# Kernel optimization log

Hardware: AMD Instinct MI355X
Metric: run time of the kernel (lower is better)

The kernel has to match this reference:

```python
import jax, jax.numpy as jnp
import numpy as np

BN_EPS = 1e-5

def conv1x1(x, w, b):
    # x: [B, Cin, L], w: [Cout, Cin], b: [Cout] -> [B, Cout, L]
    return jnp.einsum('bcl,oc->bol', x, w) + b[None, :, None]

def maxpool2(x):
    # x: [B, C, L] -> [B, C, L//2], kernel=stride=2
    B, C, L = x.shape
    return x.reshape(B, C, L // 2, 2).max(axis=-1)

def setup_inputs() -> dict:
    key = jax.random.key(0)
    ks = jax.random.split(key, 12)
    B, C, L = 8, 512, 4096
    Ci = C // 2
    s_in = 1.0 / np.sqrt(C)
    s_mid = 1.0 / np.sqrt(Ci)
    return {
        'x':       jax.random.normal(ks[0], (B, C, L), jnp.float32),
        'theta_w': jax.random.uniform(ks[1], (Ci, C), jnp.float32, -s_in, s_in),
        'theta_b': jax.random.uniform(ks[2], (Ci,), jnp.float32, -s_in, s_in),
        'phi_w':   jax.random.uniform(ks[3], (Ci, C), jnp.float32, -s_in, s_in),
        'phi_b':   jax.random.uniform(ks[4], (Ci,), jnp.float32, -s_in, s_in),
        'g_w':     jax.random.uniform(ks[5], (Ci, C), jnp.float32, -s_in, s_in),
        'g_b':     jax.random.uniform(ks[6], (Ci,), jnp.float32, -s_in, s_in),
        'wz_w':    jax.random.uniform(ks[7], (C, Ci), jnp.float32, -s_mid, s_mid),
        'wz_b':    jax.random.uniform(ks[8], (C,), jnp.float32, -s_mid, s_mid),
        'bn_gamma': jax.random.normal(ks[9], (C,), jnp.float32),
        'bn_beta':  jax.random.normal(ks[10], (C,), jnp.float32),
    }

def reference(x, theta_w, theta_b, phi_w, phi_b, g_w, g_b, wz_w, wz_b, bn_gamma, bn_beta):
    B, C, L = x.shape
    Ci = C // 2
    # projections
    theta = conv1x1(x, theta_w, theta_b)                 # [B, Ci, L]
    phi   = maxpool2(conv1x1(x, phi_w, phi_b))           # [B, Ci, L/2]
    g     = maxpool2(conv1x1(x, g_w, g_b))               # [B, Ci, L/2]
    # non-local attention (unscaled)
    f = jnp.einsum('bcq,bck->bqk', theta, phi)           # [B, L, L/2]
    f = jax.nn.softmax(f, axis=-1)
    y = jnp.einsum('bqk,bck->bcq', f, g)                 # [B, Ci, L]
    # wz: conv1x1 + BatchNorm1d (training mode: batch stats, biased var)
    z = conv1x1(y, wz_w, wz_b)                           # [B, C, L]
    mean = z.mean(axis=(0, 2))
    var = ((z - mean[None, :, None]) ** 2).mean(axis=(0, 2))
    z_hat = (z - mean[None, :, None]) * jax.lax.rsqrt(var + BN_EPS)[None, :, None]
    wz = z_hat * bn_gamma[None, :, None] + bn_beta[None, :, None]
    return wz + x
```

## Files before the change

kernel.cpp:

```cpp
#include <hip/hip_runtime.h>

#define BATCH 8
#define CIN   512
#define LEN   4096
#define CI    256
#define KLEN  2048

typedef _Float16 half_t;
typedef _Float16 half2_t __attribute__((ext_vector_type(2)));
typedef _Float16 half4_t __attribute__((ext_vector_type(4)));
typedef _Float16 half8_t __attribute__((ext_vector_type(8)));
typedef float    floatx4 __attribute__((ext_vector_type(4)));

__device__ __forceinline__ void async16(void* lds_dst, const void* g_src) {
    __builtin_amdgcn_global_load_lds(
        (const __attribute__((address_space(1))) unsigned int*)g_src,
        (__attribute__((address_space(3))) unsigned int*)lds_dst,
        16, 0, 0);
}

__global__ __launch_bounds__(256) void xpose_kernel(
    const float* __restrict__ x, half_t* __restrict__ xhT)
{
    __shared__ half_t tile[64][72];
    const int b = blockIdx.z, c0 = blockIdx.y * 64, l0 = blockIdx.x * 64;
    const int t = threadIdx.x;
    #pragma unroll
    for (int i = 0; i < 4; i++) {
        int fid = t + 256 * i;
        int c = fid >> 4, lb = (fid & 15) << 2;
        float4 v = *(const float4*)(x + ((size_t)b * CIN + c0 + c) * LEN + l0 + lb);
        tile[lb + 0][c] = (half_t)v.x;
        tile[lb + 1][c] = (half_t)v.y;
        tile[lb + 2][c] = (half_t)v.z;
        tile[lb + 3][c] = (half_t)v.w;
    }
    __syncthreads();
    #pragma unroll
    for (int i = 0; i < 2; i++) {
        int fid = t + 256 * i;
        int l = fid >> 3, cb = (fid & 7) << 3;
        half8_t v = *(const half8_t*)&tile[l][cb];
        *(half8_t*)(xhT + ((size_t)b * LEN + l0 + l) * CIN + c0 + cb) = v;
    }
}

__global__ __launch_bounds__(256) void wconv_kernel(
    const float* __restrict__ tw, const float* __restrict__ pw,
    const float* __restrict__ gw, const float* __restrict__ wzw,
    half_t* __restrict__ Wh, half_t* __restrict__ wzh)
{
    size_t base = ((size_t)blockIdx.x * 256 + threadIdx.x) * 8;
    const float* src;
    half_t* dst;
    if (base < 768 * 512) {
        size_t o = base >> 9, c = base & 511;
        src = (o < 256 ? tw + o * 512
                       : (o < 512 ? pw + (o - 256) * 512 : gw + (o - 512) * 512)) + c;
        dst = Wh + base;
    } else {
        size_t off = base - 768 * 512;
        src = wzw + off;
        dst = wzh + off;
    }
    float4 a = *(const float4*)src, b2 = *(const float4*)(src + 4);
    half8_t h = { (half_t)a.x, (half_t)a.y, (half_t)a.z, (half_t)a.w,
                  (half_t)b2.x, (half_t)b2.y, (half_t)b2.z, (half_t)b2.w };
    *(half8_t*)dst = h;
}

__global__ __launch_bounds__(256, 2) void projmm_kernel(
    const half_t* __restrict__ xhT, const half_t* __restrict__ Wh,
    const float* __restrict__ tb, const float* __restrict__ pb,
    const float* __restrict__ gb,
    half_t* __restrict__ thetaT, half_t* __restrict__ phiT,
    half_t* __restrict__ gH)
{
    __shared__ half_t wsm[128 * 32];
    __shared__ half_t xsm[128 * 32];

    const int b  = blockIdx.z;
    const int o0 = blockIdx.y * 128;
    const int l0 = blockIdx.x * 128;
    const int t  = threadIdx.x;
    const int lane = t & 63, w = t >> 6;
    const int ln = lane & 15, quad = lane >> 4;
    const int wm = w >> 1, wn = w & 1;

    floatx4 acc[4][4];
    #pragma unroll
    for (int mi = 0; mi < 4; mi++)
        #pragma unroll
        for (int nj = 0; nj < 4; nj++) acc[mi][nj] = (floatx4)(0.0f);

    const half_t* Wb = Wh + (size_t)o0 * 512;
    const half_t* xb = xhT + ((size_t)b * LEN + l0) * CIN;

    for (int k0 = 0; k0 < 512; k0 += 32) {
        __syncthreads();
        #pragma unroll
        for (int it = 0; it < 2; it++) {
            int off = t * 16 + it * 4096;
            int row = off >> 6, c8 = (off >> 4) & 3;
            async16(&wsm[off >> 1], Wb + (size_t)row * 512 + k0 + c8 * 8);
            async16(&xsm[off >> 1], xb + (size_t)row * CIN + k0 + c8 * 8);
        }
        __syncthreads();
        half8_t af[4], bf[4];
        #pragma unroll
        for (int mi = 0; mi < 4; mi++)
            af[mi] = *(const half8_t*)&wsm[(wm * 64 + mi * 16 + ln) * 32 + quad * 8];
        #pragma unroll
        for (int nj = 0; nj < 4; nj++)
            bf[nj] = *(const half8_t*)&xsm[(wn * 64 + nj * 16 + ln) * 32 + quad * 8];
        #pragma unroll
        for (int mi = 0; mi < 4; mi++)
            #pragma unroll
            for (int nj = 0; nj < 4; nj++)
                acc[mi][nj] = __builtin_amdgcn_mfma_f32_16x16x32_f16(
                                  af[mi], bf[nj], acc[mi][nj], 0, 0, 0);
    }

    const int which = o0 >> 8;
    const int obase = o0 & 255;
    const float* Bp = which == 0 ? tb : (which == 1 ? pb : gb);

    float bias[4][4];
    #pragma unroll
    for (int mi = 0; mi < 4; mi++)
        #pragma unroll
        for (int r = 0; r < 4; r++)
            bias[mi][r] = Bp[obase + wm * 64 + mi * 16 + quad * 4 + r];

    if (which == 0) {
        #pragma unroll
        for (int mi = 0; mi < 4; mi++) {
            int o = obase + wm * 64 + mi * 16 + quad * 4;
            #pragma unroll
            for (int nj = 0; nj < 4; nj++) {
                int l = l0 + wn * 64 + nj * 16 + ln;
                half4_t v = { (half_t)(acc[mi][nj][0] + bias[mi][0]),
                              (half_t)(acc[mi][nj][1] + bias[mi][1]),
                              (half_t)(acc[mi][nj][2] + bias[mi][2]),
                              (half_t)(acc[mi][nj][3] + bias[mi][3]) };
                *(half4_t*)(thetaT + ((size_t)b * LEN + l) * CI + o) = v;
            }
        }
    } else {
        #pragma unroll
        for (int mi = 0; mi < 4; mi++) {
            int o = obase + wm * 64 + mi * 16 + quad * 4;
            #pragma unroll
            for (int nj = 0; nj < 4; nj++) {
                int l = l0 + wn * 64 + nj * 16 + ln;
                float mx[4];
                #pragma unroll
                for (int r = 0; r < 4; r++) {
                    float other = __shfl_xor(acc[mi][nj][r], 1);
                    mx[r] = fmaxf(acc[mi][nj][r], other) + bias[mi][r];
                }
                if ((ln & 1) == 0) {
                    int kk = l >> 1;
                    if (which == 1) {
                        half4_t v = { (half_t)mx[0], (half_t)mx[1],
                                      (half_t)mx[2], (half_t)mx[3] };
                        *(half4_t*)(phiT + ((size_t)b * KLEN + kk) * CI + o) = v;
                    } else {
                        #pragma unroll
                        for (int r = 0; r < 4; r++)
                            gH[((size_t)b * CI + o + r) * KLEN + kk] = (half_t)mx[r];
                    }
                }
            }
        }
    }
}

__global__ __launch_bounds__(256, 2) void attn_kernel(
    const half_t* __restrict__ thetaT,
    const half_t* __restrict__ phiT,
    const half_t* __restrict__ gH,
    half_t* __restrict__ yhT)
{
    __shared__ half_t phi_s[64 * 256];
    __shared__ half_t g_s[256 * 64];

    const int b    = blockIdx.x;
    const int q0   = blockIdx.y * 64;
    const int t    = threadIdx.x;
    const int w    = t >> 6;
    const int lane = t & 63;
    const int ln   = lane & 15;
    const int quad = lane >> 4;
    const int qw   = q0 + w * 16;

    half8_t thf[8];
    {
        const half_t* thb = thetaT + ((size_t)b * LEN + qw + ln) * CI + quad * 8;
        #pragma unroll
        for (int ch = 0; ch < 8; ch++)
            thf[ch] = *(const half8_t*)(thb + ch * 32);
    }

    floatx4 O[16];
    #pragma unroll
    for (int i = 0; i < 16; i++) O[i] = (floatx4)(0.0f);
    float m_run = -3.0e38f;
    float l_run = 0.0f;

    const half_t* phib = phiT + (size_t)b * KLEN * CI;
    const half_t* gb   = gH   + (size_t)b * CI * KLEN;

    for (int kt = 0; kt < KLEN; kt += 64) {
        __syncthreads();
        #pragma unroll
        for (int it = 0; it < 8; it++) {
            int o   = t * 16 + it * 4096;
            int row = o >> 9;
            int gsw = (o >> 4) & 31;
            int gsrc = gsw ^ (row & 31);
            async16(&phi_s[o >> 1],
                    phib + (size_t)(kt + row) * CI + gsrc * 8);
        }
        #pragma unroll
        for (int it = 0; it < 8; it++) {
            int o   = t * 16 + it * 4096;
            int row = o >> 7;
            int gsw = (o >> 4) & 7;
            int gsrc = gsw ^ (row & 7);
            async16(&g_s[o >> 1],
                    gb + (size_t)row * KLEN + kt + gsrc * 8);
        }
        __syncthreads();

        floatx4 S[4];
        #pragma unroll
        for (int k16 = 0; k16 < 4; k16++) S[k16] = (floatx4)(0.0f);
        #pragma unroll
        for (int k16 = 0; k16 < 4; k16++) {
            int row = k16 * 16 + ln;
            int rs  = row & 31;
            #pragma unroll
            for (int ch = 0; ch < 8; ch++) {
                int gr = (ch * 4 + quad) ^ rs;
                half8_t a = *(const half8_t*)&phi_s[(row << 8) + gr * 8];
                S[k16] = __builtin_amdgcn_mfma_f32_16x16x32_f16(
                             a, thf[ch], S[k16], 0, 0, 0);
            }
        }

        float tmax = S[0][0];
        #pragma unroll
        for (int k16 = 0; k16 < 4; k16++)
            #pragma unroll
            for (int r = 0; r < 4; r++) tmax = fmaxf(tmax, S[k16][r]);
        tmax = fmaxf(tmax, __shfl_xor(tmax, 16));
        tmax = fmaxf(tmax, __shfl_xor(tmax, 32));
        float m_new = fmaxf(m_run, tmax);
        float alpha = __expf(m_run - m_new);
        m_run = m_new;
        l_run *= alpha;

        half4_t P[4];
        #pragma unroll
        for (int k16 = 0; k16 < 4; k16++) {
            float p0 = __expf(S[k16][0] - m_new);
            float p1 = __expf(S[k16][1] - m_new);
            float p2 = __expf(S[k16][2] - m_new);
            float p3 = __expf(S[k16][3] - m_new);
            l_run += (p0 + p1) + (p2 + p3);
            half4_t pv = { (half_t)p0, (half_t)p1, (half_t)p2, (half_t)p3 };
            P[k16] = pv;
        }
        #pragma unroll
        for (int i = 0; i < 16; i++) O[i] *= alpha;

        const int lnm = ln & 7;
        #pragma unroll
        for (int k16 = 0; k16 < 4; k16++) {
            int gr   = (2 * k16 + (quad >> 1)) ^ lnm;
            int coff = gr * 8 + (quad & 1) * 4;
            #pragma unroll
            for (int csub = 0; csub < 16; csub++) {
                int row = csub * 16 + ln;
                half4_t a = *(const half4_t*)&g_s[(row << 6) + coff];
                O[csub] = __builtin_amdgcn_mfma_f32_16x16x16f16(
                              a, P[k16], O[csub], 0, 0, 0);
            }
        }
    }

    l_run += __shfl_xor(l_run, 16);
    l_run += __shfl_xor(l_run, 32);
    float inv = 1.0f / l_run;
    half_t* yb = yhT + ((size_t)b * LEN + qw + ln) * CI;
    #pragma unroll
    for (int csub = 0; csub < 16; csub++) {
        int c = csub * 16 + quad * 4;
        half4_t v = { (half_t)(O[csub][0] * inv), (half_t)(O[csub][1] * inv),
                      (half_t)(O[csub][2] * inv), (half_t)(O[csub][3] * inv) };
        *(half4_t*)(yb + c) = v;
    }
}

__global__ __launch_bounds__(256, 2) void zmm_kernel(
    const half_t* __restrict__ yhT, const half_t* __restrict__ wzh,
    const float* __restrict__ wzb, float* __restrict__ z,
    float* __restrict__ bns, float* __restrict__ bnq)
{
    __shared__ half_t ysm[128 * 32];
    __shared__ half_t wsm[128 * 32];

    const int b  = blockIdx.z;
    const int o0 = blockIdx.y * 128;
    const int l0 = blockIdx.x * 128;
    const int t  = threadIdx.x;
    const int lane = t & 63, w = t >> 6;
    const int ln = lane & 15, quad = lane >> 4;
    const int wm = w >> 1, wn = w & 1;

    floatx4 acc[4][4];
    #pragma unroll
    for (int mi = 0; mi < 4; mi++)
        #pragma unroll
        for (int nj = 0; nj < 4; nj++) acc[mi][nj] = (floatx4)(0.0f);

    const half_t* yb = yhT + ((size_t)b * LEN + l0) * CI;
    const half_t* Wb = wzh + (size_t)o0 * CI;

    for (int k0 = 0; k0 < 256; k0 += 32) {
        __syncthreads();
        #pragma unroll
        for (int it = 0; it < 2; it++) {
            int off = t * 16 + it * 4096;
            int row = off >> 6, c8 = (off >> 4) & 3;
            async16(&ysm[off >> 1], yb + (size_t)row * CI + k0 + c8 * 8);
            async16(&wsm[off >> 1], Wb + (size_t)row * CI + k0 + c8 * 8);
        }
        __syncthreads();
        half8_t af[4], bf[4];
        #pragma unroll
        for (int mi = 0; mi < 4; mi++)
            af[mi] = *(const half8_t*)&ysm[(wm * 64 + mi * 16 + ln) * 32 + quad * 8];
        #pragma unroll
        for (int nj = 0; nj < 4; nj++)
            bf[nj] = *(const half8_t*)&wsm[(wn * 64 + nj * 16 + ln) * 32 + quad * 8];
        #pragma unroll
        for (int mi = 0; mi < 4; mi++)
            #pragma unroll
            for (int nj = 0; nj < 4; nj++)
                acc[mi][nj] = __builtin_amdgcn_mfma_f32_16x16x32_f16(
                                  af[mi], bf[nj], acc[mi][nj], 0, 0, 0);
    }

    float s[4] = {0, 0, 0, 0}, s2[4] = {0, 0, 0, 0};
    #pragma unroll
    for (int nj = 0; nj < 4; nj++) {
        int o = o0 + wn * 64 + nj * 16 + ln;
        float bo = wzb[o];
        #pragma unroll
        for (int mi = 0; mi < 4; mi++) {
            int l = l0 + wm * 64 + mi * 16 + quad * 4;
            float4 v = make_float4(acc[mi][nj][0] + bo, acc[mi][nj][1] + bo,
                                   acc[mi][nj][2] + bo, acc[mi][nj][3] + bo);
            *(float4*)(z + ((size_t)b * CIN + o) * LEN + l) = v;
            s[nj]  += (v.x + v.y) + (v.z + v.w);
            s2[nj] += (v.x * v.x + v.y * v.y) + (v.z * v.z + v.w * v.w);
        }
    }
    #pragma unroll
    for (int nj = 0; nj < 4; nj++) {
        float sv = s[nj], qv = s2[nj];
        sv += __shfl_xor(sv, 16); sv += __shfl_xor(sv, 32);
        qv += __shfl_xor(qv, 16); qv += __shfl_xor(qv, 32);
        if (quad == 0) {
            int o = o0 + wn * 64 + nj * 16 + ln;
            atomicAdd(&bns[o], sv);
            atomicAdd(&bnq[o], qv);
        }
    }
}

__global__ __launch_bounds__(256) void bn_kernel(
    float* __restrict__ z, const float* __restrict__ x,
    const float* __restrict__ bns, const float* __restrict__ bnq,
    const float* __restrict__ gamma, const float* __restrict__ beta)
{
    size_t i4 = (size_t)blockIdx.x * 256 + threadIdx.x;
    size_t base = i4 << 2;
    int c = (int)((base >> 12) & (CIN - 1));
    const float invn = 1.0f / (BATCH * LEN);
    float mean = bns[c] * invn;
    float var  = bnq[c] * invn - mean * mean;
    float sc = gamma[c] * rsqrtf(var + 1e-5f);
    float sh = beta[c] - mean * sc;
    float4 zv = *(const float4*)(z + base);
    float4 xv = *(const float4*)(x + base);
    float4 o;
    o.x = zv.x * sc + sh + xv.x;
    o.y = zv.y * sc + sh + xv.y;
    o.z = zv.z * sc + sh + xv.z;
    o.w = zv.w * sc + sh + xv.w;
    *(float4*)(z + base) = o;
}

extern "C" void kernel_launch(void* const* d_in, const int* in_sizes, int n_in,
                              void* d_out, int out_size, void* d_ws, size_t ws_size,
                              hipStream_t stream)
{
    const float* x     = (const float*)d_in[0];
    const float* tw    = (const float*)d_in[1];
    const float* tb    = (const float*)d_in[2];
    const float* pw    = (const float*)d_in[3];
    const float* pb    = (const float*)d_in[4];
    const float* gw    = (const float*)d_in[5];
    const float* gb    = (const float*)d_in[6];
    const float* wzw   = (const float*)d_in[7];
    const float* wzb   = (const float*)d_in[8];
    const float* gamma = (const float*)d_in[9];
    const float* beta  = (const float*)d_in[10];

    float* out = (float*)d_out;

    half_t* xhT    = (half_t*)d_ws;
    half_t* thetaT = xhT    + (size_t)BATCH * LEN * CIN;
    half_t* phiT   = thetaT + (size_t)BATCH * LEN * CI;
    half_t* gH     = phiT   + (size_t)BATCH * KLEN * CI;
    half_t* yhT    = gH     + (size_t)BATCH * CI * KLEN;
    half_t* Wh     = yhT    + (size_t)BATCH * LEN * CI;
    half_t* wzh    = Wh     + (size_t)768 * 512;
    float*  bns    = (float*)(wzh + (size_t)512 * 256);
    float*  bnq    = bns + CIN;

    hipMemsetAsync(bns, 0, 2 * CIN * sizeof(float), stream);

    wconv_kernel<<<256, 256, 0, stream>>>(tw, pw, gw, wzw, Wh, wzh);

    xpose_kernel<<<dim3(LEN / 64, CIN / 64, BATCH), 256, 0, stream>>>(x, xhT);

    projmm_kernel<<<dim3(LEN / 128, 6, BATCH), 256, 0, stream>>>(
        xhT, Wh, tb, pb, gb, thetaT, phiT, gH);

    attn_kernel<<<dim3(BATCH, LEN / 64), 256, 0, stream>>>(
        thetaT, phiT, gH, yhT);

    zmm_kernel<<<dim3(LEN / 128, CIN / 128, BATCH), 256, 0, stream>>>(
        yhT, wzh, wzb, out, bns, bnq);

    bn_kernel<<<(BATCH * CIN * LEN) / 4 / 256, 256, 0, stream>>>(
        out, x, bns, bnq, gamma, beta);
}
```

Baseline: 332.9 us.

## Process two query tiles per wave in attention to reuse LDS K/V tiles

Each wave in the attention kernel now handles 32 query rows, two 16-row sub-tiles, instead of 16, so each block covers 128 queries and the grid is halved. Each phi/g fragment read from LDS feeds two MFMAs, which halves LDS and global traffic per query. The cost is roughly double the accumulator and theta registers (O grows to 2x16 floatx4). Under launch_bounds(256,2) that may cause spills or lower occupancy, and only 256 blocks are launched.

```diff
diff --git a/kernel.cpp b/kernel.cpp
--- a/kernel.cpp
+++ b/kernel.cpp
@@ -186,27 +186,30 @@
     __shared__ half_t g_s[256 * 64];
 
     const int b    = blockIdx.x;
-    const int q0   = blockIdx.y * 64;
+    const int q0   = blockIdx.y * 128;
     const int t    = threadIdx.x;
     const int w    = t >> 6;
     const int lane = t & 63;
     const int ln   = lane & 15;
     const int quad = lane >> 4;
-    const int qw   = q0 + w * 16;
-
-    half8_t thf[8];
-    {
-        const half_t* thb = thetaT + ((size_t)b * LEN + qw + ln) * CI + quad * 8;
+    const int qw   = q0 + w * 32;
+
+    half8_t thf[2][8];
+    #pragma unroll
+    for (int u = 0; u < 2; u++) {
+        const half_t* thb = thetaT + ((size_t)b * LEN + qw + u * 16 + ln) * CI + quad * 8;
         #pragma unroll
         for (int ch = 0; ch < 8; ch++)
-            thf[ch] = *(const half8_t*)(thb + ch * 32);
-    }
-
-    floatx4 O[16];
-    #pragma unroll
-    for (int i = 0; i < 16; i++) O[i] = (floatx4)(0.0f);
-    float m_run = -3.0e38f;
-    float l_run = 0.0f;
+            thf[u][ch] = *(const half8_t*)(thb + ch * 32);
+    }
+
+    floatx4 O[2][16];
+    #pragma unroll
+    for (int u = 0; u < 2; u++)
+        #pragma unroll
+        for (int i = 0; i < 16; i++) O[u][i] = (floatx4)(0.0f);
+    float m_run[2] = { -3.0e38f, -3.0e38f };
+    float l_run[2] = { 0.0f, 0.0f };
 
     const half_t* phib = phiT + (size_t)b * KLEN * CI;
     const half_t* gb   = gH   + (size_t)b * CI * KLEN;
@@ -233,9 +236,11 @@
         }
         __syncthreads();
 
-        floatx4 S[4];
-        #pragma unroll
-        for (int k16 = 0; k16 < 4; k16++) S[k16] = (floatx4)(0.0f);
+        floatx4 S[2][4];
+        #pragma unroll
+        for (int u = 0; u < 2; u++)
+            #pragma unroll
+            for (int k16 = 0; k16 < 4; k16++) S[u][k16] = (floatx4)(0.0f);
         #pragma unroll
         for (int k16 = 0; k16 < 4; k16++) {
             int row = k16 * 16 + ln;
@@ -244,36 +249,41 @@
             for (int ch = 0; ch < 8; ch++) {
                 int gr = (ch * 4 + quad) ^ rs;
                 half8_t a = *(const half8_t*)&phi_s[(row << 8) + gr * 8];
-                S[k16] = __builtin_amdgcn_mfma_f32_16x16x32_f16(
-                             a, thf[ch], S[k16], 0, 0, 0);
+                S[0][k16] = __builtin_amdgcn_mfma_f32_16x16x32_f16(
+                                a, thf[0][ch], S[0][k16], 0, 0, 0);
+                S[1][k16] = __builtin_amdgcn_mfma_f32_16x16x32_f16(
+                                a, thf[1][ch], S[1][k16], 0, 0, 0);
             }
         }
 
-        float tmax = S[0][0];
-        #pragma unroll
-        for (int k16 = 0; k16 < 4; k16++)
-            #pragma unroll
-            for (int r = 0; r < 4; r++) tmax = fmaxf(tmax, S[k16][r]);
-        tmax = fmaxf(tmax, __shfl_xor(tmax, 16));
-        tmax = fmaxf(tmax, __shfl_xor(tmax, 32));
-        float m_new = fmaxf(m_run, tmax);
-        float alpha = __expf(m_run - m_new);
-        m_run = m_new;
-        l_run *= alpha;
-
-        half4_t P[4];
-        #pragma unroll
-        for (int k16 = 0; k16 < 4; k16++) {
-            float p0 = __expf(S[k16][0] - m_new);
-            float p1 = __expf(S[k16][1] - m_new);
-            float p2 = __expf(S[k16][2] - m_new);
-            float p3 = __expf(S[k16][3] - m_new);
-            l_run += (p0 + p1) + (p2 + p3);
-            half4_t pv = { (half_t)p0, (half_t)p1, (half_t)p2, (half_t)p3 };
-            P[k16] = pv;
-        }
-        #pragma unroll
-        for (int i = 0; i < 16; i++) O[i] *= alpha;
+        half4_t P[2][4];
+        #pragma unroll
+        for (int u = 0; u < 2; u++) {
+            float tmax = S[u][0][0];
+            #pragma unroll
+            for (int k16 = 0; k16 < 4; k16++)
+                #pragma unroll
+                for (int r = 0; r < 4; r++) tmax = fmaxf(tmax, S[u][k16][r]);
+            tmax = fmaxf(tmax, __shfl_xor(tmax, 16));
+            tmax = fmaxf(tmax, __shfl_xor(tmax, 32));
+            float m_new = fmaxf(m_run[u], tmax);
+            float alpha = __expf(m_run[u] - m_new);
+            m_run[u] = m_new;
+            l_run[u] *= alpha;
+
+            #pragma unroll
+            for (int k16 = 0; k16 < 4; k16++) {
+                float p0 = __expf(S[u][k16][0] - m_new);
+                float p1 = __expf(S[u][k16][1] - m_new);
+                float p2 = __expf(S[u][k16][2] - m_new);
+                float p3 = __expf(S[u][k16][3] - m_new);
+                l_run[u] += (p0 + p1) + (p2 + p3);
+                half4_t pv = { (half_t)p0, (half_t)p1, (half_t)p2, (half_t)p3 };
+                P[u][k16] = pv;
+            }
+            #pragma unroll
+            for (int i = 0; i < 16; i++) O[u][i] *= alpha;
+        }
 
         const int lnm = ln & 7;
         #pragma unroll
@@ -284,22 +294,28 @@
             for (int csub = 0; csub < 16; csub++) {
                 int row = csub * 16 + ln;
                 half4_t a = *(const half4_t*)&g_s[(row << 6) + coff];
-                O[csub] = __builtin_amdgcn_mfma_f32_16x16x16f16(
-                              a, P[k16], O[csub], 0, 0, 0);
+                O[0][csub] = __builtin_amdgcn_mfma_f32_16x16x16f16(
+                                 a, P[0][k16], O[0][csub], 0, 0, 0);
+                O[1][csub] = __builtin_amdgcn_mfma_f32_16x16x16f16(
+                                 a, P[1][k16], O[1][csub], 0, 0, 0);
             }
         }
     }
 
-    l_run += __shfl_xor(l_run, 16);
-    l_run += __shfl_xor(l_run, 32);
-    float inv = 1.0f / l_run;
-    half_t* yb = yhT + ((size_t)b * LEN + qw + ln) * CI;
-    #pragma unroll
-    for (int csub = 0; csub < 16; csub++) {
-        int c = csub * 16 + quad * 4;
-        half4_t v = { (half_t)(O[csub][0] * inv), (half_t)(O[csub][1] * inv),
-                      (half_t)(O[csub][2] * inv), (half_t)(O[csub][3] * inv) };
-        *(half4_t*)(yb + c) = v;
+    #pragma unroll
+    for (int u = 0; u < 2; u++) {
+        float lr = l_run[u];
+        lr += __shfl_xor(lr, 16);
+        lr += __shfl_xor(lr, 32);
+        float inv = 1.0f / lr;
+        half_t* yb = yhT + ((size_t)b * LEN + qw + u * 16 + ln) * CI;
+        #pragma unroll
+        for (int csub = 0; csub < 16; csub++) {
+            int c = csub * 16 + quad * 4;
+            half4_t v = { (half_t)(O[u][csub][0] * inv), (half_t)(O[u][csub][1] * inv),
+                          (half_t)(O[u][csub][2] * inv), (half_t)(O[u][csub][3] * inv) };
+            *(half4_t*)(yb + c) = v;
+        }
     }
 }
 
@@ -441,7 +457,7 @@
     projmm_kernel<<<dim3(LEN / 128, 6, BATCH), 256, 0, stream>>>(
         xhT, Wh, tb, pb, gb, thetaT, phiT, gH);
 
-    attn_kernel<<<dim3(BATCH, LEN / 64), 256, 0, stream>>>(
+    attn_kernel<<<dim3(BATCH, LEN / 128), 256, 0, stream>>>(
         thetaT, phiT, gH, yhT);
 
     zmm_kernel<<<dim3(LEN / 128, CIN / 128, BATCH), 256, 0, stream>>>(
```

New measurement: 412.7 us. 24.0% more time.
